# Optimization experiments

Measured on AMD Instinct MI355X. Metric: run time of the kernel, lower is better.

The kernel has to match this reference:

```python
import jax, jax.numpy as jnp
import numpy as np

E, N, HID, NH = 250000, 50000, 128, 4
HD = HID // NH  # head_dim = 32


def setup_inputs() -> dict:
    key = jax.random.key(0)
    ks = jax.random.split(key, 16)
    f = lambda k, s: jax.random.normal(k, s, dtype=jnp.float32)
    w = lambda k, s: jax.random.normal(k, s, dtype=jnp.float32) * 0.05
    return {
        "edge_attr": f(ks[0], (E, HID)),
        "node_features": f(ks[1], (N, HID)),
        "regime_probs": jax.random.uniform(ks[2], (3,), dtype=jnp.float32),
        # phase_query / phase_key: Linear(hidden+3 -> hidden)
        "Wq": w(ks[3], (HID, HID + 3)), "bq": jnp.zeros((HID,), jnp.float32),
        "Wk": w(ks[4], (HID, HID + 3)), "bk": jnp.zeros((HID,), jnp.float32),
        # phase_value: Linear(hidden -> hidden)
        "Wv": w(ks[5], (HID, HID)), "bv": jnp.zeros((HID,), jnp.float32),
        # nn.MultiheadAttention packed in-projection [3*hid, hid] and out_proj
        "W_in": w(ks[6], (3 * HID, HID)), "b_in": jnp.zeros((3 * HID,), jnp.float32),
        "W_mo": w(ks[7], (HID, HID)), "b_mo": jnp.zeros((HID,), jnp.float32),
        # output_proj
        "Wo": w(ks[8], (HID, HID)), "bo": jnp.zeros((HID,), jnp.float32),
        "edge_index": jax.random.randint(ks[9], (2, E), 0, N, dtype=jnp.int64),
    }


def reference(edge_attr, node_features, regime_probs,
              Wq, bq, Wk, bk, Wv, bv,
              W_in, b_in, W_mo, b_mo, Wo, bo,
              edge_index):
    e = edge_attr.shape[0]
    src = node_features[edge_index[0]]  # [E, HID] gather
    tgt = node_features[edge_index[1]]  # [E, HID] gather
    reg = jnp.broadcast_to(regime_probs, (e, regime_probs.shape[0]))  # [E, 3]

    q = jnp.concatenate([src, reg], axis=1) @ Wq.T + bq  # [E, HID]
    k = jnp.concatenate([tgt, reg], axis=1) @ Wk.T + bk  # [E, HID]
    v = edge_attr @ Wv.T + bv                             # [E, HID]

    # nn.MultiheadAttention with seq_len 1 (batch_first): in-proj, heads, softmax, out-proj
    Wiq, Wik, Wiv = jnp.split(W_in, 3, axis=0)
    biq, bik, biv = jnp.split(b_in, 3)
    q2 = (q @ Wiq.T + biq).reshape(e, NH, HD)
    k2 = (k @ Wik.T + bik).reshape(e, NH, HD)
    v2 = (v @ Wiv.T + biv).reshape(e, NH, HD)

    scale = 1.0 / jnp.sqrt(jnp.float32(HD))
    scores = jnp.sum(q2 * k2, axis=-1, keepdims=True) * scale  # [E, NH, 1]
    probs = jax.nn.softmax(scores, axis=-1)                    # seq-len-1 -> all ones
    att = (probs * v2).reshape(e, HID)                         # == v2 merged
    att = att @ W_mo.T + b_mo                                  # MHA out_proj

    out = att @ Wo.T + bo                                      # output_proj
    return edge_attr + 0.5 * out
```

## Files before the change

kernel.cpp:

```cpp
#include <hip/hip_runtime.h>
#include <hip/hip_bf16.h>

#define HID 128

typedef __attribute__((ext_vector_type(8))) short short8;
typedef __attribute__((ext_vector_type(4))) float f32x4;

static __device__ __forceinline__ short f2bf(float x) {
    __hip_bfloat16 h = __float2bfloat16(x);
    return *reinterpret_cast<short*>(&h);
}

__global__ void prep_products(const float* __restrict__ Wo,
                              const float* __restrict__ W_mo,
                              const float* __restrict__ Wiv,
                              const float* __restrict__ Wv,
                              const float* __restrict__ bv,
                              const float* __restrict__ biv,
                              const float* __restrict__ b_mo,
                              const float* __restrict__ bo,
                              float* __restrict__ Pl,
                              float* __restrict__ Pr,
                              float* __restrict__ cv)
{
    const int j = threadIdx.x;
    const int b = blockIdx.x;
    __shared__ float sh[HID];

    if (b < 256) {
        const float* A = (b < 128) ? Wo   : Wiv;
        const float* B = (b < 128) ? W_mo : Wv;
        float*       C = (b < 128) ? Pl   : Pr;
        const int i = b & 127;
        sh[j] = A[i * HID + j];
        __syncthreads();
        float s = 0.f;
        #pragma unroll 16
        for (int k = 0; k < HID; ++k) s += sh[k] * B[k * HID + j];
        C[i * HID + j] = s;
    } else {
        sh[j] = bv[j];
        __syncthreads();
        float t = biv[j];
        #pragma unroll 16
        for (int k = 0; k < HID; ++k) t += Wiv[j * HID + k] * sh[k];
        __syncthreads(); sh[j] = t; __syncthreads();
        t = b_mo[j];
        #pragma unroll 16
        for (int k = 0; k < HID; ++k) t += W_mo[j * HID + k] * sh[k];
        __syncthreads(); sh[j] = t; __syncthreads();
        t = bo[j];
        #pragma unroll 16
        for (int k = 0; k < HID; ++k) t += Wo[j * HID + k] * sh[k];
        cv[j] = 0.5f * t;
    }
}

__global__ void prep_final(const float* __restrict__ Pl,
                           const float* __restrict__ Pr,
                           __hip_bfloat16* __restrict__ Mb)
{
    const int i = blockIdx.x, j = threadIdx.x;
    __shared__ float sh[HID];
    sh[j] = Pl[i * HID + j];
    __syncthreads();
    float s = 0.f;
    #pragma unroll 16
    for (int k = 0; k < HID; ++k) s += sh[k] * Pr[k * HID + j];
    Mb[i * HID + j] = __float2bfloat16(((i == j) ? 1.0f : 0.0f) + 0.5f * s);
}

__global__ __launch_bounds__(256) void edge_gemm(
    const float* __restrict__ ea,
    const __hip_bfloat16* __restrict__ Mb,
    const float* __restrict__ cvec,
    float* __restrict__ out,
    int E, int numTiles)
{
    __shared__ __align__(16) float lds[2][2048];

    const int lane  = threadIdx.x & 63;
    const int wv    = threadIdx.x >> 6;
    const int q     = lane >> 4;
    const int c     = lane & 15;
    const int ncol0 = wv * 32;

    short8 Mfrag[2][4];
    #pragma unroll
    for (int nt = 0; nt < 2; ++nt) {
        const __hip_bfloat16* mp = Mb + (size_t)(ncol0 + nt * 16 + c) * HID + q * 8;
        #pragma unroll
        for (int kk = 0; kk < 4; ++kk)
            Mfrag[nt][kk] = *reinterpret_cast<const short8*>(mp + kk * 32);
    }
    f32x4 cvp[2];
    #pragma unroll
    for (int nt = 0; nt < 2; ++nt)
        cvp[nt] = *reinterpret_cast<const f32x4*>(cvec + ncol0 + nt * 16 + q * 4);

    int t = blockIdx.x;
    if (t >= numTiles) return;

    const int swz   = (c & 7) << 4;
    const int rbase = c * 512 + ((q * 32) ^ (swz & 0x60));
    const int hx    = swz & 16;

    auto stage_tile = [&](float* ldsbuf, int edge0) {
        #pragma unroll
        for (int j = 0; j < 2; ++j) {
            const int i = wv * 2 + j;
            const int r = i * 2 + (lane >> 5);
            const int b = ((lane & 31) * 16) ^ ((r & 7) << 4);
            int grow = edge0 + r; if (grow > E - 1) grow = E - 1;
            const char* src = (const char*)ea + (size_t)grow * 512 + b;
            float* dst = ldsbuf + i * 256;
            __builtin_amdgcn_global_load_lds(
                (const __attribute__((address_space(1))) void*)src,
                (__attribute__((address_space(3))) void*)dst,
                16, 0, 0);
        }
    };

    stage_tile(&lds[0][0], t * 16);
    asm volatile("s_waitcnt vmcnt(0)" ::: "memory");
    __builtin_amdgcn_s_barrier();
    __builtin_amdgcn_sched_barrier(0);

    int cur = 0;
    while (true) {
        const int edge0 = t * 16;
        const int tn    = t + gridDim.x;
        const bool has_next = (tn < numTiles);

        if (has_next) stage_tile(&lds[cur ^ 1][0], tn * 16);

        const char* lb = (const char*)&lds[cur][0];
        short8 bfrag[4];
        #pragma unroll
        for (int kk = 0; kk < 4; ++kk) {
            const float4 f0 = *reinterpret_cast<const float4*>(lb + rbase + kk * 128 + hx);
            const float4 f1 = *reinterpret_cast<const float4*>(lb + rbase + kk * 128 + (16 ^ hx));
            short8 v;
            v[0] = f2bf(f0.x); v[1] = f2bf(f0.y); v[2] = f2bf(f0.z); v[3] = f2bf(f0.w);
            v[4] = f2bf(f1.x); v[5] = f2bf(f1.y); v[6] = f2bf(f1.z); v[7] = f2bf(f1.w);
            bfrag[kk] = v;
        }

        f32x4 acc[2] = { cvp[0], cvp[1] };
        #pragma unroll
        for (int kk = 0; kk < 4; ++kk) {
            acc[0] = __builtin_amdgcn_mfma_f32_16x16x32_bf16(Mfrag[0][kk], bfrag[kk], acc[0], 0, 0, 0);
            acc[1] = __builtin_amdgcn_mfma_f32_16x16x32_bf16(Mfrag[1][kk], bfrag[kk], acc[1], 0, 0, 0);
        }

        const int orow = edge0 + c;
        if (orow < E) {
            float* op = out + (size_t)orow * HID + ncol0 + q * 4;
            __builtin_nontemporal_store(acc[0], reinterpret_cast<f32x4*>(op));
            __builtin_nontemporal_store(acc[1], reinterpret_cast<f32x4*>(op + 16));
        }

        if (!has_next) break;

        asm volatile("s_waitcnt vmcnt(2)" ::: "memory");
        __builtin_amdgcn_s_barrier();
        __builtin_amdgcn_sched_barrier(0);

        cur ^= 1;
        t = tn;
    }
}

extern "C" void kernel_launch(void* const* d_in, const int* in_sizes, int n_in,
                              void* d_out, int out_size, void* d_ws, size_t ws_size,
                              hipStream_t stream) {
    const float* Wv   = (const float*)d_in[7];
    const float* bv   = (const float*)d_in[8];
    const float* W_in = (const float*)d_in[9];
    const float* b_in = (const float*)d_in[10];
    const float* W_mo = (const float*)d_in[11];
    const float* b_mo = (const float*)d_in[12];
    const float* Wo   = (const float*)d_in[13];
    const float* bo   = (const float*)d_in[14];
    const float* Wiv  = W_in + 2 * HID * HID;
    const float* biv  = b_in + 2 * HID;

    char* ws = (char*)d_ws;
    float*          Pl = (float*)(ws);
    float*          Pr = (float*)(ws + 65536);
    __hip_bfloat16* Mb = (__hip_bfloat16*)(ws + 131072);
    float*          cv = (float*)(ws + 163840);

    const int E = in_sizes[0] / HID;
    const int numTiles = (E + 15) / 16;
    const int grid = numTiles < 2048 ? numTiles : 2048;

    prep_products<<<dim3(257), dim3(HID), 0, stream>>>(
        Wo, W_mo, Wiv, Wv, bv, biv, b_mo, bo, Pl, Pr, cv);
    prep_final<<<dim3(HID), dim3(HID), 0, stream>>>(Pl, Pr, Mb);

    edge_gemm<<<dim3(grid), dim3(256), 0, stream>>>(
        (const float*)d_in[0], Mb, cv, (float*)d_out, E, numTiles);
}
```

Before: 283.7 us.

## Give each wave its own edge tile with private double-buffered LDS

Each wave now owns a whole 16-edge tile and computes all 128 output columns, holding the full M matrix in registers. Staging uses a private per-wave LDS double buffer, so the block-wide barriers go away. The grid is fixed at 512 blocks, i.e. 2048 waves striding over tiles. The aim is to remove workgroup synchronisation stalls and let each wave stream on its own, at the cost of many more registers (32 M fragments plus 8 accumulators) and a larger LDS footprint. Output stores also switch from nontemporal to ordinary stores.

```diff
diff --git a/kernel.cpp b/kernel.cpp
--- a/kernel.cpp
+++ b/kernel.cpp
@@ -75,45 +75,46 @@
     const __hip_bfloat16* __restrict__ Mb,
     const float* __restrict__ cvec,
     float* __restrict__ out,
-    int E, int numTiles)
+    int E, int numTiles, int nwaves)
 {
-    __shared__ __align__(16) float lds[2][2048];
-
-    const int lane  = threadIdx.x & 63;
-    const int wv    = threadIdx.x >> 6;
-    const int q     = lane >> 4;
-    const int c     = lane & 15;
-    const int ncol0 = wv * 32;
-
-    short8 Mfrag[2][4];
+    __shared__ __align__(16) float lds[4][2][2048];
+
+    const int lane = threadIdx.x & 63;
+    const int wv   = threadIdx.x >> 6;
+    const int q    = lane >> 4;
+    const int c    = lane & 15;
+
+    short8 Mfrag[8][4];
     #pragma unroll
-    for (int nt = 0; nt < 2; ++nt) {
-        const __hip_bfloat16* mp = Mb + (size_t)(ncol0 + nt * 16 + c) * HID + q * 8;
+    for (int nt = 0; nt < 8; ++nt) {
+        const __hip_bfloat16* mp = Mb + (size_t)(nt * 16 + c) * HID + q * 8;
         #pragma unroll
         for (int kk = 0; kk < 4; ++kk)
             Mfrag[nt][kk] = *reinterpret_cast<const short8*>(mp + kk * 32);
     }
-    f32x4 cvp[2];
+    f32x4 cvp[8];
     #pragma unroll
-    for (int nt = 0; nt < 2; ++nt)
-        cvp[nt] = *reinterpret_cast<const f32x4*>(cvec + ncol0 + nt * 16 + q * 4);
-
-    int t = blockIdx.x;
+    for (int nt = 0; nt < 8; ++nt)
+        cvp[nt] = *reinterpret_cast<const f32x4*>(cvec + nt * 16 + q * 4);
+
+    int t = blockIdx.x * 4 + wv;
     if (t >= numTiles) return;
 
     const int swz   = (c & 7) << 4;
     const int rbase = c * 512 + ((q * 32) ^ (swz & 0x60));
     const int hx    = swz & 16;
 
-    auto stage_tile = [&](float* ldsbuf, int edge0) {
-        #pragma unroll
-        for (int j = 0; j < 2; ++j) {
-            const int i = wv * 2 + j;
+    float* bufA = &lds[wv][0][0];
+    float* bufB = &lds[wv][1][0];
+
+    auto stage = [&](float* buf, int edge0) {
+        #pragma unroll
+        for (int i = 0; i < 8; ++i) {
             const int r = i * 2 + (lane >> 5);
             const int b = ((lane & 31) * 16) ^ ((r & 7) << 4);
             int grow = edge0 + r; if (grow > E - 1) grow = E - 1;
             const char* src = (const char*)ea + (size_t)grow * 512 + b;
-            float* dst = ldsbuf + i * 256;
+            float* dst = buf + i * 256;
             __builtin_amdgcn_global_load_lds(
                 (const __attribute__((address_space(1))) void*)src,
                 (__attribute__((address_space(3))) void*)dst,
@@ -121,21 +122,11 @@
         }
     };
 
-    stage_tile(&lds[0][0], t * 16);
-    asm volatile("s_waitcnt vmcnt(0)" ::: "memory");
-    __builtin_amdgcn_s_barrier();
-    __builtin_amdgcn_sched_barrier(0);
-
-    int cur = 0;
-    while (true) {
-        const int edge0 = t * 16;
-        const int tn    = t + gridDim.x;
-        const bool has_next = (tn < numTiles);
-
-        if (has_next) stage_tile(&lds[cur ^ 1][0], tn * 16);
-
-        const char* lb = (const char*)&lds[cur][0];
-        short8 bfrag[4];
+    auto compute_store = [&](const float* buf, int tt) {
+        f32x4 acc[8];
+        #pragma unroll
+        for (int nt = 0; nt < 8; ++nt) acc[nt] = cvp[nt];
+        const char* lb = (const char*)buf;
         #pragma unroll
         for (int kk = 0; kk < 4; ++kk) {
             const float4 f0 = *reinterpret_cast<const float4*>(lb + rbase + kk * 128 + hx);
@@ -143,30 +134,47 @@
             short8 v;
             v[0] = f2bf(f0.x); v[1] = f2bf(f0.y); v[2] = f2bf(f0.z); v[3] = f2bf(f0.w);
             v[4] = f2bf(f1.x); v[5] = f2bf(f1.y); v[6] = f2bf(f1.z); v[7] = f2bf(f1.w);
-            bfrag[kk] = v;
+            #pragma unroll
+            for (int nt = 0; nt < 8; ++nt)
+                acc[nt] = __builtin_amdgcn_mfma_f32_16x16x32_bf16(Mfrag[nt][kk], v, acc[nt], 0, 0, 0);
         }
-
-        f32x4 acc[2] = { cvp[0], cvp[1] };
-        #pragma unroll
-        for (int kk = 0; kk < 4; ++kk) {
-            acc[0] = __builtin_amdgcn_mfma_f32_16x16x32_bf16(Mfrag[0][kk], bfrag[kk], acc[0], 0, 0, 0);
-            acc[1] = __builtin_amdgcn_mfma_f32_16x16x32_bf16(Mfrag[1][kk], bfrag[kk], acc[1], 0, 0, 0);
+        const int orow = tt * 16 + c;
+        if (orow < E) {
+            float* op = out + (size_t)orow * HID + q * 4;
+            #pragma unroll
+            for (int nt = 0; nt < 8; ++nt)
+                *reinterpret_cast<f32x4*>(op + nt * 16) = acc[nt];
         }
-
-        const int orow = edge0 + c;
-        if (orow < E) {
-            float* op = out + (size_t)orow * HID + ncol0 + q * 4;
-            __builtin_nontemporal_store(acc[0], reinterpret_cast<f32x4*>(op));
-            __builtin_nontemporal_store(acc[1], reinterpret_cast<f32x4*>(op + 16));
-        }
+    };
+
+    stage(bufA, t * 16);
+    const int t2 = t + nwaves;
+    const bool has2 = (t2 < numTiles);
+    if (has2) stage(bufB, t2 * 16);
+
+    if (has2) { asm volatile("s_waitcnt vmcnt(8)" ::: "memory"); }
+    else      { asm volatile("s_waitcnt vmcnt(0)" ::: "memory"); }
+    __builtin_amdgcn_sched_barrier(0);
+    compute_store(bufA, t);
+    if (!has2) return;
+
+    float* curb = bufB;
+    float* othb = bufA;
+    t = t2;
+    while (true) {
+        const int tn = t + nwaves;
+        const bool has_next = (tn < numTiles);
+
+        if (has_next) stage(othb, tn * 16);
+
+        if (has_next) { asm volatile("s_waitcnt vmcnt(16)" ::: "memory"); }
+        else          { asm volatile("s_waitcnt vmcnt(8)"  ::: "memory"); }
+        __builtin_amdgcn_sched_barrier(0);
+
+        compute_store(curb, t);
 
         if (!has_next) break;
-
-        asm volatile("s_waitcnt vmcnt(2)" ::: "memory");
-        __builtin_amdgcn_s_barrier();
-        __builtin_amdgcn_sched_barrier(0);
-
-        cur ^= 1;
+        float* tmp = curb; curb = othb; othb = tmp;
         t = tn;
     }
 }
@@ -193,12 +201,14 @@
 
     const int E = in_sizes[0] / HID;
     const int numTiles = (E + 15) / 16;
-    const int grid = numTiles < 2048 ? numTiles : 2048;
+
+    const int nblocks = 512;
+    const int nwaves  = nblocks * 4;
 
     prep_products<<<dim3(257), dim3(HID), 0, stream>>>(
         Wo, W_mo, Wiv, Wv, bv, biv, b_mo, bo, Pl, Pr, cv);
     prep_final<<<dim3(HID), dim3(HID), 0, stream>>>(Pl, Pr, Mb);
 
-    edge_gemm<<<dim3(grid), dim3(256), 0, stream>>>(
-        (const float*)d_in[0], Mb, cv, (float*)d_out, E, numTiles);
-}
+    edge_gemm<<<dim3(nblocks), dim3(256), 0, stream>>>(
+        (const float*)d_in[0], Mb, cv, (float*)d_out, E, numTiles, nwaves);
+}
```

Result: no change. 287.7 us (+1.4%).

## Stage edge tiles through registers with two-deep prefetch instead of direct-to-LDS loads

Applied to the files above, without the earlier changes.

Replaces the global_load_lds staging with ordinary vector loads into registers. Two tiles are kept in flight per thread, written into alternating swizzled LDS buffers, and separated by an LDS-count wait plus a barrier. The aim is deeper memory-level parallelism and a wait on LDS writes only, rather than on the global load counter. Output stores also switch from nontemporal to regular stores, which changes cache behaviour for the streamed result. The cost is more registers in use and extra LDS write instructions.

```diff
diff --git a/kernel.cpp b/kernel.cpp
--- a/kernel.cpp
+++ b/kernel.cpp
@@ -100,42 +100,38 @@
 
     int t = blockIdx.x;
     if (t >= numTiles) return;
+    const int G = gridDim.x;
+
+    const int ldrow = threadIdx.x >> 4;
+    const int ldoff = (threadIdx.x & 15) * 32;
+    const int wsw  = (ldrow & 7) << 4;
+    const int wad0 = ldrow * 512 + (ldoff ^ wsw);
+    const int wad1 = wad0 ^ 16;
 
     const int swz   = (c & 7) << 4;
     const int rbase = c * 512 + ((q * 32) ^ (swz & 0x60));
     const int hx    = swz & 16;
 
-    auto stage_tile = [&](float* ldsbuf, int edge0) {
-        #pragma unroll
-        for (int j = 0; j < 2; ++j) {
-            const int i = wv * 2 + j;
-            const int r = i * 2 + (lane >> 5);
-            const int b = ((lane & 31) * 16) ^ ((r & 7) << 4);
-            int grow = edge0 + r; if (grow > E - 1) grow = E - 1;
-            const char* src = (const char*)ea + (size_t)grow * 512 + b;
-            float* dst = ldsbuf + i * 256;
-            __builtin_amdgcn_global_load_lds(
-                (const __attribute__((address_space(1))) void*)src,
-                (__attribute__((address_space(3))) void*)dst,
-                16, 0, 0);
-        }
-    };
-
-    stage_tile(&lds[0][0], t * 16);
-    asm volatile("s_waitcnt vmcnt(0)" ::: "memory");
-    __builtin_amdgcn_s_barrier();
-    __builtin_amdgcn_sched_barrier(0);
-
-    int cur = 0;
-    while (true) {
-        const int edge0 = t * 16;
-        const int tn    = t + gridDim.x;
-        const bool has_next = (tn < numTiles);
-
-        if (has_next) stage_tile(&lds[cur ^ 1][0], tn * 16);
-
-        const char* lb = (const char*)&lds[cur][0];
-        short8 bfrag[4];
+    auto load_tile = [&](int tt, float4& r0, float4& r1) {
+        int row = tt * 16 + ldrow; if (row > E - 1) row = E - 1;
+        const char* p = (const char*)ea + (size_t)row * 512 + ldoff;
+        r0 = *reinterpret_cast<const float4*>(p);
+        r1 = *reinterpret_cast<const float4*>(p + 16);
+    };
+    auto write_tile = [&](int buf, const float4& r0, const float4& r1) {
+        char* lb = (char*)&lds[buf][0];
+        *reinterpret_cast<float4*>(lb + wad0) = r0;
+        *reinterpret_cast<float4*>(lb + wad1) = r1;
+    };
+    auto sync = [&]() {
+        __builtin_amdgcn_sched_barrier(0);
+        asm volatile("s_waitcnt lgkmcnt(0)" ::: "memory");
+        __builtin_amdgcn_s_barrier();
+        __builtin_amdgcn_sched_barrier(0);
+    };
+    auto compute_store = [&](int buf, int tt) {
+        const char* lb = (const char*)&lds[buf][0];
+        f32x4 acc[2] = { cvp[0], cvp[1] };
         #pragma unroll
         for (int kk = 0; kk < 4; ++kk) {
             const float4 f0 = *reinterpret_cast<const float4*>(lb + rbase + kk * 128 + hx);
@@ -143,31 +139,37 @@
             short8 v;
             v[0] = f2bf(f0.x); v[1] = f2bf(f0.y); v[2] = f2bf(f0.z); v[3] = f2bf(f0.w);
             v[4] = f2bf(f1.x); v[5] = f2bf(f1.y); v[6] = f2bf(f1.z); v[7] = f2bf(f1.w);
-            bfrag[kk] = v;
+            acc[0] = __builtin_amdgcn_mfma_f32_16x16x32_bf16(Mfrag[0][kk], v, acc[0], 0, 0, 0);
+            acc[1] = __builtin_amdgcn_mfma_f32_16x16x32_bf16(Mfrag[1][kk], v, acc[1], 0, 0, 0);
         }
-
-        f32x4 acc[2] = { cvp[0], cvp[1] };
-        #pragma unroll
-        for (int kk = 0; kk < 4; ++kk) {
-            acc[0] = __builtin_amdgcn_mfma_f32_16x16x32_bf16(Mfrag[0][kk], bfrag[kk], acc[0], 0, 0, 0);
-            acc[1] = __builtin_amdgcn_mfma_f32_16x16x32_bf16(Mfrag[1][kk], bfrag[kk], acc[1], 0, 0, 0);
-        }
-
-        const int orow = edge0 + c;
+        const int orow = tt * 16 + c;
         if (orow < E) {
             float* op = out + (size_t)orow * HID + ncol0 + q * 4;
-            __builtin_nontemporal_store(acc[0], reinterpret_cast<f32x4*>(op));
-            __builtin_nontemporal_store(acc[1], reinterpret_cast<f32x4*>(op + 16));
+            *reinterpret_cast<f32x4*>(op)      = acc[0];
+            *reinterpret_cast<f32x4*>(op + 16) = acc[1];
         }
-
-        if (!has_next) break;
-
-        asm volatile("s_waitcnt vmcnt(2)" ::: "memory");
-        __builtin_amdgcn_s_barrier();
-        __builtin_amdgcn_sched_barrier(0);
-
-        cur ^= 1;
-        t = tn;
+    };
+
+    float4 a0, a1, b0, b1;
+    load_tile(t, a0, a1);
+    bool hB = (t + G < numTiles);
+    if (hB) load_tile(t + G, b0, b1);
+
+    while (true) {
+        write_tile(0, a0, a1);
+        if (t + 2 * G < numTiles) load_tile(t + 2 * G, a0, a1);
+        sync();
+        compute_store(0, t);
+        if (!hB) break;
+
+        write_tile(1, b0, b1);
+        if (t + 3 * G < numTiles) load_tile(t + 3 * G, b0, b1);
+        sync();
+        compute_store(1, t + G);
+
+        t += 2 * G;
+        if (t >= numTiles) break;
+        hB = (t + G < numTiles);
     }
 }
 
```

New measurement: 278.7 us. About the same (-1.8%).
